# Optimization experiments

Measured on AMD Instinct MI355X. Metric: run time of the kernel, lower is better.

The kernel has to match this reference:

```python
import jax, jax.numpy as jnp
import numpy as np

N_NODES = 100_000
N_EDGES = 1_000_000
H = 128
NUM_STATES = 4
UPPER_T, LOWER_T, NUM_ITERS, TEMP_EVAL = 1.0, 0.1, 10000, 0.1


def temp_by_step(step, upper, lower, num_iters, temp_eval):
    # Python-level schedule: eval temp at step == -1, else linear anneal.
    if step == -1:
        return temp_eval
    frac = min(step / num_iters, 1.0)
    return upper + (lower - upper) * frac


def from_binary_states(states):
    # [*, k] bits -> integer id in [0, 2**k)
    weights = 2 ** jnp.arange(states.shape[-1])
    return (states * weights).sum(-1)


def setup_inputs() -> dict:
    key = jax.random.key(0)
    ks = jax.random.split(key, 20)
    N, E, h = N_NODES, N_EDGES, H
    node_states = jax.random.randint(ks[0], (N, NUM_STATES), 0, 2)
    edge_states = jax.random.randint(ks[1], (E, NUM_STATES), 0, 2)
    scalars = jax.random.normal(ks[2], (E, 1), jnp.float32)
    # first N edges are self-loops ordered by node id (required by the module's
    # node_scalars = scalars[src == dst] indexing convention)
    loops = jnp.arange(N)
    src = jax.random.randint(ks[3], (E - N,), 0, N)
    dst = jax.random.randint(ks[4], (E - N,), 0, N)
    dst = jnp.where(dst == src, (dst + 1) % N, dst)  # no accidental self-loops
    edge_index = jnp.stack([jnp.concatenate([loops, src]),
                            jnp.concatenate([loops, dst])])
    batched_reverse_idx = jax.random.randint(ks[5], (E,), 0, E)
    batch_scalars = jax.random.normal(ks[6], (E, 1, 1), jnp.float32)
    s = 0.02
    params = dict(
        node_emb=s * jax.random.normal(ks[7], (2 ** NUM_STATES, h), jnp.float32),
        edge_emb=s * jax.random.normal(ks[8], (2 ** NUM_STATES, h), jnp.float32),
        combine_W=s * jax.random.normal(ks[9], (2 * h, h), jnp.float32),
        combine_b=jnp.zeros((h,), jnp.float32),
        keep_W=s * jax.random.normal(ks[10], (h, 2), jnp.float32),
        keep_b=jnp.zeros((2,), jnp.float32),
        push_W=s * jax.random.normal(ks[11], (h, 2), jnp.float32),
        push_b=jnp.zeros((2,), jnp.float32),
        push_node_W=s * jax.random.normal(ks[12], (h, 2), jnp.float32),
        push_node_b=jnp.zeros((2,), jnp.float32),
        increment_W=s * jax.random.normal(ks[13], (h, 2), jnp.float32),
        increment_b=jnp.zeros((2,), jnp.float32),
    )
    return dict(node_states=node_states, edge_states=edge_states, scalars=scalars,
                edge_index=edge_index, batched_reverse_idx=batched_reverse_idx,
                batch_scalars=batch_scalars, processor_step=0, training_step=0,
                **params)


def reference(node_states, edge_states, scalars, edge_index, batched_reverse_idx,
              batch_scalars, processor_step, training_step,
              node_emb, edge_emb, combine_W, combine_b, keep_W, keep_b,
              push_W, push_b, push_node_W, push_node_b,
              increment_W, increment_b):
    N = node_states.shape[0]
    tau = temp_by_step(int(training_step), UPPER_T, LOWER_T, NUM_ITERS, TEMP_EVAL)
    # use_noise = config.use_noise (False) and training_step != -1 -> False

    node_fts = node_emb[from_binary_states(node_states)]   # [N, h]
    edge_fts = edge_emb[from_binary_states(edge_states)]   # [E, h]
    src, dst = edge_index[0], edge_index[1]
    fts = jnp.concatenate([edge_fts[batched_reverse_idx], node_fts[src]], axis=1)
    fts = fts @ combine_W + combine_b                       # [E, h]

    s = scalars.reshape(-1)                                 # [E]

    def pair_gumbel_first(W, b):
        # grouped (per-edge pair) softmax; take first component (== [::2])
        logits = (fts @ W + b) / tau                        # [E, 2]
        return jax.nn.softmax(logits, axis=-1)[:, 0]

    increment = 1.0 * pair_gumbel_first(increment_W, increment_b)
    keep = s * pair_gumbel_first(keep_W, keep_b)

    # push: first N edges are self-loops, self-loop of node i is edge i
    push_wo = pair_gumbel_first(push_W, push_b)
    push_w = pair_gumbel_first(push_node_W, push_node_b)
    node_scalars = s[:N]                                    # scalars at self-loops
    s_wo = s - node_scalars[dst]
    s_w = s_wo + node_scalars[src]
    acc = (jax.ops.segment_sum(push_wo * s_wo, dst, num_segments=N)
           + jax.ops.segment_sum(push_w * s_w, dst, num_segments=N))  # [N]
    edge_push = jnp.zeros_like(s).at[:N].set(acc)           # nonzero only on self-loops

    new_scalars = (increment + keep + edge_push)[:, None]   # [E, 1]
    target = batch_scalars[:, processor_step]               # [E, 1]
    loss = jnp.mean((target - new_scalars) ** 2)
    return new_scalars, loss
```

## Files before the change

### kernel.cpp

```cpp
#include <hip/hip_runtime.h>
#include <math.h>

#define N_NODES 100000
#define N_EDGES 1000000
#define HDIM 128
#define N_NONLOOP (N_EDGES - N_NODES)

typedef float  vfloat2 __attribute__((ext_vector_type(2)));
typedef float  vfloat4 __attribute__((ext_vector_type(4)));

__device__ __forceinline__ float get_invtau(const int* __restrict__ training_step) {
    int step = training_step[0];
    float tau;
    if (step == -1) {
        tau = 0.1f;
    } else {
        float frac = fminf((float)step / 10000.0f, 1.0f);
        tau = 1.0f + (0.1f - 1.0f) * frac;
    }
    return 1.0f / tau;
}

__device__ __forceinline__ float wave_reduce(float v) {
    #pragma unroll
    for (int off = 32; off > 0; off >>= 1) v += __shfl_down(v, off, 64);
    return v;
}

__global__ void tab_stage1(const float* __restrict__ cW,
                           const float* __restrict__ kW, const float* __restrict__ pW,
                           const float* __restrict__ pnW, const float* __restrict__ iW,
                           const int* __restrict__ tstep,
                           float* __restrict__ uv)
{
    __shared__ float wd[512];
    const float invtau = get_invtau(tstep);
    for (int i = threadIdx.x; i < 512; i += 256) {
        const int h = i >> 7, d = i & 127;
        const float* W = (h == 0) ? kW : (h == 1) ? pW : (h == 2) ? pnW : iW;
        wd[i] = W[2 * d] - W[2 * d + 1];
    }
    __syncthreads();

    const int row  = blockIdx.x * 4 + (threadIdx.x >> 6);
    const int lane = threadIdx.x & 63;
    const int half = row >> 9;
    const int r    = row & 511;
    const int h    = r >> 7, d = r & 127;
    const int cwrow = half * 128 + d;

    float p = cW[cwrow * 128 + lane]      * wd[h * 128 + lane]
            + cW[cwrow * 128 + 64 + lane] * wd[h * 128 + 64 + lane];
    p = wave_reduce(p);
    if (lane == 0) uv[row] = p * invtau;
}

__global__ void tab_stage2(const float* __restrict__ node_emb,
                           const float* __restrict__ edge_emb,
                           const float* __restrict__ cb,
                           const float* __restrict__ kW, const float* __restrict__ kb,
                           const float* __restrict__ pW, const float* __restrict__ pb,
                           const float* __restrict__ pnW, const float* __restrict__ pnb,
                           const float* __restrict__ iW, const float* __restrict__ ib,
                           const int* __restrict__ tstep,
                           const float* __restrict__ uv,
                           float* __restrict__ tabs)
{
    const int w = blockIdx.x * 4 + (threadIdx.x >> 6);
    if (w >= 132) return;
    const int lane = threadIdx.x & 63;
    const float invtau = get_invtau(tstep);

    float p;
    if (w < 128) {
        const int isB = w >> 6, h = (w >> 4) & 3, i = w & 15;
        const float* emb = isB ? node_emb : edge_emb;
        const float* uvp = uv + isB * 512 + h * 128;
        p = emb[i * 128 + lane] * uvp[lane] + emb[i * 128 + 64 + lane] * uvp[64 + lane];
    } else {
        const int h = w - 128;
        const float* W = (h == 0) ? kW : (h == 1) ? pW : (h == 2) ? pnW : iW;
        p = cb[lane]      * (W[2 * lane] - W[2 * lane + 1])
          + cb[64 + lane] * (W[2 * (64 + lane)] - W[2 * (64 + lane) + 1]);
    }
    p = wave_reduce(p);
    if (lane == 0) {
        if (w < 64) {
            const int h = (w >> 4) & 3, i = w & 15;
            tabs[i * 4 + h] = p;
        } else if (w < 128) {
            const int h = (w >> 4) & 3, i = w & 15;
            tabs[64 + i * 4 + h] = p;
        } else {
            const int h = w - 128;
            const float* b = (h == 0) ? kb : (h == 1) ? pb : (h == 2) ? pnb : ib;
            tabs[128 + h] = (p + b[0] - b[1]) * invtau;
        }
    }
}

__global__ void precompute(const int* __restrict__ node_states,
                           const int* __restrict__ edge_states,
                           unsigned char* __restrict__ es_idx,
                           unsigned char* __restrict__ ns_idx,
                           float* __restrict__ acc,
                           float* __restrict__ loss_out)
{
    const int e = blockIdx.x * blockDim.x + threadIdx.x;
    if (e < N_EDGES) {
        int4 st = ((const int4*)edge_states)[e];
        es_idx[e] = (unsigned char)(st.x + 2 * st.y + 4 * st.z + 8 * st.w);
    }
    if (e < N_NODES) {
        int4 st = ((const int4*)node_states)[e];
        ns_idx[e] = (unsigned char)(st.x + 2 * st.y + 4 * st.z + 8 * st.w);
        acc[e] = 0.f;
    }
    if (e == 0) *loss_out = 0.f;
}

__global__ __launch_bounds__(256) void edge_kernel(
    const float* __restrict__ s,
    const int* __restrict__ src,
    const int* __restrict__ dst,
    const int* __restrict__ brev,
    const unsigned char* __restrict__ es_idx,
    const unsigned char* __restrict__ ns_idx,
    const float* __restrict__ tabs,
    const float* __restrict__ target,
    float* __restrict__ acc,
    float* __restrict__ out,
    float* __restrict__ loss_out)
{
    __shared__ float4 sf[33];
    if (threadIdx.x < 33) sf[threadIdx.x] = ((const float4*)tabs)[threadIdx.x];
    __syncthreads();

    const int t = blockIdx.x * blockDim.x + threadIdx.x;
    float lsum = 0.f;

    if (t < N_NONLOOP / 2) {
        const int g = (N_NODES / 2) + t;
        const int2   rv = ((const int2*)brev)[g];
        const int2   sr = ((const int2*)src)[g];
        const int2   ds = ((const int2*)dst)[g];
        const float2 sv = ((const float2*)s)[g];
        const float2 tg = ((const float2*)target)[g];

        const int rvv[2] = {rv.x, rv.y};
        const int srv[2] = {sr.x, sr.y};
        const int dsv[2] = {ds.x, ds.y};
        const float svv[2] = {sv.x, sv.y};
        const float tgv[2] = {tg.x, tg.y};

        int ei[2], ni[2];
        float sd[2], ss[2];
        #pragma unroll
        for (int j = 0; j < 2; ++j) {
            ei[j] = es_idx[rvv[j]];
            ni[j] = ns_idx[srv[j]];
            sd[j] = s[dsv[j]];
            ss[j] = s[srv[j]];
        }

        const float4 c4 = sf[32];
        float ov[2];
        #pragma unroll
        for (int j = 0; j < 2; ++j) {
            const float4 a = sf[ei[j]];
            const float4 b = sf[16 + ni[j]];
            const float lk  = a.x + b.x + c4.x;
            const float lp  = a.y + b.y + c4.y;
            const float lpn = a.z + b.z + c4.z;
            const float li  = a.w + b.w + c4.w;
            const float pk  = 1.f / (1.f + __expf(-lk));
            const float pp  = 1.f / (1.f + __expf(-lp));
            const float ppn = 1.f / (1.f + __expf(-lpn));
            const float pi  = 1.f / (1.f + __expf(-li));

            const float s_wo = svv[j] - sd[j];
            const float s_w  = s_wo + ss[j];
            unsafeAtomicAdd(&acc[dsv[j]], pp * s_wo + ppn * s_w);

            ov[j] = pi + svv[j] * pk;
            const float d = tgv[j] - ov[j];
            lsum += d * d;
        }
        vfloat2 o2 = {ov[0], ov[1]};
        __builtin_nontemporal_store(o2, &((vfloat2*)out)[g]);
    }

    lsum = wave_reduce(lsum);
    __shared__ float wsum[4];
    const int lane = threadIdx.x & 63, wid = threadIdx.x >> 6;
    if (lane == 0) wsum[wid] = lsum;
    __syncthreads();
    if (threadIdx.x == 0) {
        const float tot = wsum[0] + wsum[1] + wsum[2] + wsum[3];
        atomicAdd(loss_out, tot * (1.0f / (float)N_EDGES));
    }
}

__global__ __launch_bounds__(256) void finalize_nodes(
    const float* __restrict__ s,
    const int* __restrict__ brev,
    const unsigned char* __restrict__ es_idx,
    const unsigned char* __restrict__ ns_idx,
    const float* __restrict__ tabs,
    const float* __restrict__ target,
    const float* __restrict__ acc,
    float* __restrict__ out,
    float* __restrict__ loss_out)
{
    __shared__ float4 sf[33];
    if (threadIdx.x < 33) sf[threadIdx.x] = ((const float4*)tabs)[threadIdx.x];
    __syncthreads();

    const int n = blockIdx.x * blockDim.x + threadIdx.x;
    float sq = 0.f;
    if (n < N_NODES) {
        const int   rev = brev[n];
        const int   ei  = es_idx[rev];
        const int   ni  = ns_idx[n];
        const float sv  = s[n];

        const float4 a = sf[ei];
        const float4 b = sf[16 + ni];
        const float4 c4 = sf[32];
        const float lk  = a.x + b.x + c4.x;
        const float lpn = a.z + b.z + c4.z;
        const float li  = a.w + b.w + c4.w;
        const float pk  = 1.f / (1.f + __expf(-lk));
        const float ppn = 1.f / (1.f + __expf(-lpn));
        const float pi  = 1.f / (1.f + __expf(-li));

        const float v = pi + sv * pk + ppn * sv + acc[n];
        out[n] = v;
        const float d = target[n] - v;
        sq = d * d;
    }
    sq = wave_reduce(sq);
    __shared__ float wsum[4];
    const int lane = threadIdx.x & 63, wid = threadIdx.x >> 6;
    if (lane == 0) wsum[wid] = sq;
    __syncthreads();
    if (threadIdx.x == 0) {
        const float tot = wsum[0] + wsum[1] + wsum[2] + wsum[3];
        atomicAdd(loss_out, tot * (1.0f / (float)N_EDGES));
    }
}

extern "C" void kernel_launch(void* const* d_in, const int* in_sizes, int n_in,
                              void* d_out, int out_size, void* d_ws, size_t ws_size,
                              hipStream_t stream) {
    const int*   node_states   = (const int*)d_in[0];
    const int*   edge_states   = (const int*)d_in[1];
    const float* scalars       = (const float*)d_in[2];
    const int*   edge_index    = (const int*)d_in[3];
    const int*   brev          = (const int*)d_in[4];
    const float* batch_scalars = (const float*)d_in[5];
    const int*   training_step = (const int*)d_in[7];
    const float* node_emb  = (const float*)d_in[8];
    const float* edge_emb  = (const float*)d_in[9];
    const float* combine_W = (const float*)d_in[10];
    const float* combine_b = (const float*)d_in[11];
    const float* keep_W  = (const float*)d_in[12];
    const float* keep_b  = (const float*)d_in[13];
    const float* push_W  = (const float*)d_in[14];
    const float* push_b  = (const float*)d_in[15];
    const float* pushn_W = (const float*)d_in[16];
    const float* pushn_b = (const float*)d_in[17];
    const float* inc_W   = (const float*)d_in[18];
    const float* inc_b   = (const float*)d_in[19];

    float* out = (float*)d_out;

    char* ws = (char*)d_ws;
    float* tabs = (float*)ws;
    float* uv   = (float*)(ws + 1024);
    float* acc  = (float*)(ws + 1024 + 4096);
    unsigned char* es_idx = (unsigned char*)(ws + 1024 + 4096 + (size_t)N_NODES * 4);
    unsigned char* ns_idx = es_idx + N_EDGES;

    const int* srcp = edge_index;
    const int* dstp = edge_index + N_EDGES;

    tab_stage1<<<256, 256, 0, stream>>>(combine_W, keep_W, push_W, pushn_W, inc_W,
                                        training_step, uv);
    tab_stage2<<<33, 256, 0, stream>>>(node_emb, edge_emb, combine_b,
                                       keep_W, keep_b, push_W, push_b,
                                       pushn_W, pushn_b, inc_W, inc_b,
                                       training_step, uv, tabs);

    precompute<<<(N_EDGES + 255) / 256, 256, 0, stream>>>(node_states, edge_states,
                                                          es_idx, ns_idx, acc,
                                                          out + N_EDGES);

    const int ethreads = N_NONLOOP / 2;
    edge_kernel<<<(ethreads + 255) / 256, 256, 0, stream>>>(
        scalars, srcp, dstp, brev, es_idx, ns_idx, tabs, batch_scalars,
        acc, out, out + N_EDGES);

    finalize_nodes<<<(N_NODES + 255) / 256, 256, 0, stream>>>(
        scalars, brev, es_idx, ns_idx, tabs, batch_scalars, acc, out, out + N_EDGES);
}
```

Measured before the change: 184.2 us.

## Pack node scalar and state index together; process four edges per thread

Precompute now writes a per-node float2 holding the scalar and the state index bit-cast into the second lane. The edge kernel then fetches the source node's scalar and state index with one random 8-byte gather instead of two separate gathers. The edge kernel also handles four edges per thread with int4/float4 loads, and reads target with a nontemporal load. Fewer random gather transactions and more memory-level parallelism per thread come at the cost of a larger node table (8 bytes per node) and fewer threads in flight.

```diff
diff --git a/kernel.cpp b/kernel.cpp
--- a/kernel.cpp
+++ b/kernel.cpp
@@ -101,8 +101,9 @@
 
 __global__ void precompute(const int* __restrict__ node_states,
                            const int* __restrict__ edge_states,
+                           const float* __restrict__ s,
                            unsigned char* __restrict__ es_idx,
-                           unsigned char* __restrict__ ns_idx,
+                           float2* __restrict__ node_pack,
                            float* __restrict__ acc,
                            float* __restrict__ loss_out)
 {
@@ -113,7 +114,11 @@
     }
     if (e < N_NODES) {
         int4 st = ((const int4*)node_states)[e];
-        ns_idx[e] = (unsigned char)(st.x + 2 * st.y + 4 * st.z + 8 * st.w);
+        const int idx = st.x + 2 * st.y + 4 * st.z + 8 * st.w;
+        float2 np;
+        np.x = s[e];
+        np.y = __int_as_float(idx);
+        node_pack[e] = np;
         acc[e] = 0.f;
     }
     if (e == 0) *loss_out = 0.f;
@@ -125,7 +130,7 @@
     const int* __restrict__ dst,
     const int* __restrict__ brev,
     const unsigned char* __restrict__ es_idx,
-    const unsigned char* __restrict__ ns_idx,
+    const float2* __restrict__ node_pack,
     const float* __restrict__ tabs,
     const float* __restrict__ target,
     float* __restrict__ acc,
@@ -139,36 +144,38 @@
     const int t = blockIdx.x * blockDim.x + threadIdx.x;
     float lsum = 0.f;
 
-    if (t < N_NONLOOP / 2) {
-        const int g = (N_NODES / 2) + t;
-        const int2   rv = ((const int2*)brev)[g];
-        const int2   sr = ((const int2*)src)[g];
-        const int2   ds = ((const int2*)dst)[g];
-        const float2 sv = ((const float2*)s)[g];
-        const float2 tg = ((const float2*)target)[g];
-
-        const int rvv[2] = {rv.x, rv.y};
-        const int srv[2] = {sr.x, sr.y};
-        const int dsv[2] = {ds.x, ds.y};
-        const float svv[2] = {sv.x, sv.y};
-        const float tgv[2] = {tg.x, tg.y};
-
-        int ei[2], ni[2];
-        float sd[2], ss[2];
+    if (t < N_NONLOOP / 4) {
+        const int g = (N_NODES / 4) + t;
+        const int4   rv = ((const int4*)brev)[g];
+        const int4   sr = ((const int4*)src)[g];
+        const int4   ds = ((const int4*)dst)[g];
+        const float4 sv = ((const float4*)s)[g];
+        const vfloat4 tg = __builtin_nontemporal_load(&((const vfloat4*)target)[g]);
+
+        const int rvv[4] = {rv.x, rv.y, rv.z, rv.w};
+        const int srv[4] = {sr.x, sr.y, sr.z, sr.w};
+        const int dsv[4] = {ds.x, ds.y, ds.z, ds.w};
+        const float svv[4] = {sv.x, sv.y, sv.z, sv.w};
+        const float tgv[4] = {tg.x, tg.y, tg.z, tg.w};
+
+        int ei[4];
+        float2 np[4];
+        float sd[4];
         #pragma unroll
-        for (int j = 0; j < 2; ++j) {
+        for (int j = 0; j < 4; ++j) {
             ei[j] = es_idx[rvv[j]];
-            ni[j] = ns_idx[srv[j]];
-            sd[j] = s[dsv[j]];
-            ss[j] = s[srv[j]];
+            np[j] = node_pack[srv[j]];
+            sd[j] = node_pack[dsv[j]].x;
         }
 
         const float4 c4 = sf[32];
-        float ov[2];
+        float ov[4];
         #pragma unroll
-        for (int j = 0; j < 2; ++j) {
+        for (int j = 0; j < 4; ++j) {
+            const int   ni = __float_as_int(np[j].y);
+            const float ss = np[j].x;
             const float4 a = sf[ei[j]];
-            const float4 b = sf[16 + ni[j]];
+            const float4 b = sf[16 + ni];
             const float lk  = a.x + b.x + c4.x;
             const float lp  = a.y + b.y + c4.y;
             const float lpn = a.z + b.z + c4.z;
@@ -179,15 +186,15 @@
             const float pi  = 1.f / (1.f + __expf(-li));
 
             const float s_wo = svv[j] - sd[j];
-            const float s_w  = s_wo + ss[j];
+            const float s_w  = s_wo + ss;
             unsafeAtomicAdd(&acc[dsv[j]], pp * s_wo + ppn * s_w);
 
             ov[j] = pi + svv[j] * pk;
             const float d = tgv[j] - ov[j];
             lsum += d * d;
         }
-        vfloat2 o2 = {ov[0], ov[1]};
-        __builtin_nontemporal_store(o2, &((vfloat2*)out)[g]);
+        vfloat4 o4 = {ov[0], ov[1], ov[2], ov[3]};
+        __builtin_nontemporal_store(o4, &((vfloat4*)out)[g]);
     }
 
     lsum = wave_reduce(lsum);
@@ -202,10 +209,9 @@
 }
 
 __global__ __launch_bounds__(256) void finalize_nodes(
-    const float* __restrict__ s,
     const int* __restrict__ brev,
     const unsigned char* __restrict__ es_idx,
-    const unsigned char* __restrict__ ns_idx,
+    const float2* __restrict__ node_pack,
     const float* __restrict__ tabs,
     const float* __restrict__ target,
     const float* __restrict__ acc,
@@ -219,10 +225,11 @@
     const int n = blockIdx.x * blockDim.x + threadIdx.x;
     float sq = 0.f;
     if (n < N_NODES) {
-        const int   rev = brev[n];
-        const int   ei  = es_idx[rev];
-        const int   ni  = ns_idx[n];
-        const float sv  = s[n];
+        const int    rev = brev[n];
+        const int    ei  = es_idx[rev];
+        const float2 np  = node_pack[n];
+        const int    ni  = __float_as_int(np.y);
+        const float  sv  = np.x;
 
         const float4 a = sf[ei];
         const float4 b = sf[16 + ni];
@@ -234,7 +241,7 @@
         const float ppn = 1.f / (1.f + __expf(-lpn));
         const float pi  = 1.f / (1.f + __expf(-li));
 
-        const float v = pi + sv * pk + ppn * sv + acc[n];
+        const float v = pi + sv * (pk + ppn) + acc[n];
         out[n] = v;
         const float d = target[n] - v;
         sq = d * d;
@@ -276,11 +283,11 @@
     float* out = (float*)d_out;
 
     char* ws = (char*)d_ws;
-    float* tabs = (float*)ws;
-    float* uv   = (float*)(ws + 1024);
-    float* acc  = (float*)(ws + 1024 + 4096);
-    unsigned char* es_idx = (unsigned char*)(ws + 1024 + 4096 + (size_t)N_NODES * 4);
-    unsigned char* ns_idx = es_idx + N_EDGES;
+    float*  tabs = (float*)ws;
+    float*  uv   = (float*)(ws + 1024);
+    float*  acc  = (float*)(ws + 1024 + 4096);
+    float2* node_pack = (float2*)(ws + 1024 + 4096 + (size_t)N_NODES * 4);
+    unsigned char* es_idx = (unsigned char*)(ws + 1024 + 4096 + (size_t)N_NODES * 12);
 
     const int* srcp = edge_index;
     const int* dstp = edge_index + N_EDGES;
@@ -293,14 +300,14 @@
                                        training_step, uv, tabs);
 
     precompute<<<(N_EDGES + 255) / 256, 256, 0, stream>>>(node_states, edge_states,
-                                                          es_idx, ns_idx, acc,
-                                                          out + N_EDGES);
-
-    const int ethreads = N_NONLOOP / 2;
+                                                          scalars, es_idx, node_pack,
+                                                          acc, out + N_EDGES);
+
+    const int ethreads = N_NONLOOP / 4;
     edge_kernel<<<(ethreads + 255) / 256, 256, 0, stream>>>(
-        scalars, srcp, dstp, brev, es_idx, ns_idx, tabs, batch_scalars,
+        scalars, srcp, dstp, brev, es_idx, node_pack, tabs, batch_scalars,
         acc, out, out + N_EDGES);
 
     finalize_nodes<<<(N_NODES + 255) / 256, 256, 0, stream>>>(
-        scalars, brev, es_idx, ns_idx, tabs, batch_scalars, acc, out, out + N_EDGES);
-}
+        brev, es_idx, node_pack, tabs, batch_scalars, acc, out, out + N_EDGES);
+}
```

Result: faster. 179.3 us (-2.7%).
